# Kernel tuning notes

Measured on AMD Instinct MI355X. Metric: run time of the kernel, lower is better.

Reference implementation:

```python
import jax, jax.numpy as jnp
import numpy as np

D_MODEL = 2048
D_COMPARE = 2048
D_MEMORY = 2048
N_HEADS = 16
KV_HEADS = 4
KV_REPEAT = N_HEADS // KV_HEADS          # 4
C_HD = D_COMPARE // N_HEADS              # 128 compare head dim
M_HD = D_MEMORY // N_HEADS               # 128 memory head dim
TOTAL_OUT = D_COMPARE + KV_HEADS * C_HD + KV_HEADS * M_HD  # 3072


def setup_inputs() -> dict:
    key = jax.random.key(0)
    ks = jax.random.split(key, 5)
    b, t = 2, 2048
    x = jax.random.normal(ks[0], (b, t, D_MODEL), dtype=jnp.float32)
    s_in = 1.0 / np.sqrt(D_MODEL)
    s_out = 1.0 / np.sqrt(D_MEMORY)
    in_w = jax.random.uniform(ks[1], (TOTAL_OUT, D_MODEL), jnp.float32, -s_in, s_in)
    in_b = jax.random.uniform(ks[2], (TOTAL_OUT,), jnp.float32, -s_in, s_in)
    out_w = jax.random.uniform(ks[3], (D_MODEL, D_MEMORY), jnp.float32, -s_out, s_out)
    out_b = jax.random.uniform(ks[4], (D_MODEL,), jnp.float32, -s_out, s_out)
    return {"x": x, "in_w": in_w, "in_b": in_b, "out_w": out_w, "out_b": out_b}


def reference(x, in_w, in_b, out_w, out_b):
    b, t, _ = x.shape
    packed = jnp.einsum("btd,od->bto", x, in_w) + in_b          # [b,t,TOTAL_OUT]
    q, k, v = jnp.split(packed, [D_COMPARE, D_COMPARE + KV_HEADS * C_HD], axis=-1)
    # q: [b, kv, rep, t, hd] -- head h maps to kv group h // KV_REPEAT
    # (torch repeat_interleave on KV head dim == grouped reshape of q heads)
    q = q.reshape(b, t, KV_HEADS, KV_REPEAT, C_HD).transpose(0, 2, 3, 1, 4)
    k = k.reshape(b, t, KV_HEADS, C_HD).transpose(0, 2, 1, 3)   # [b,kv,t,hd]
    v = v.reshape(b, t, KV_HEADS, M_HD).transpose(0, 2, 1, 3)   # [b,kv,t,mhd]
    scale = 1.0 / np.sqrt(C_HD)
    scores = jnp.einsum("bgrqd,bgkd->bgrqk", q, k) * scale      # [b,kv,rep,t,t]
    attn = jax.nn.softmax(scores, axis=-1)
    y = jnp.einsum("bgrqk,bgkd->bgrqd", attn, v)                # [b,kv,rep,t,mhd]
    y = y.transpose(0, 3, 1, 2, 4).reshape(b, t, D_MEMORY)      # heads back in order
    return jnp.einsum("btm,dm->btd", y, out_w) + out_b
```

## Files before the change

### kernel.cpp

```cpp
#include <hip/hip_runtime.h>
#include <hip/hip_bf16.h>
#include <stdint.h>

#define DEV __device__ __forceinline__

typedef __attribute__((ext_vector_type(8))) short bf16x8;
typedef __attribute__((ext_vector_type(4))) float f32x4;
typedef __attribute__((ext_vector_type(16))) float f32x16;
typedef __attribute__((ext_vector_type(4))) unsigned u32x4;

DEV unsigned short f2bf(float f) {
  unsigned u = __builtin_bit_cast(unsigned, f);
  unsigned r = u + 0x7FFF + ((u >> 16) & 1);
  return (unsigned short)(r >> 16);
}

DEV unsigned short f2bfh(float f) {
  __bf16 h = (__bf16)f;
  return __builtin_bit_cast(unsigned short, h);
}

DEV unsigned cvtpk(float lo, float hi) {
  unsigned r;
  asm("v_cvt_pk_bf16_f32 %0, %1, %2" : "=v"(r) : "v"(lo), "v"(hi));
  return r;
}

DEV void plswap(unsigned &a, unsigned &b) {
  asm("v_permlane32_swap_b32 %0, %1" : "+v"(a), "+v"(b));
}

typedef __attribute__((address_space(1))) void gvoid;
typedef __attribute__((address_space(3))) void lvoid;

DEV void g2l16(const void* g, void* l) {
  __builtin_amdgcn_global_load_lds((gvoid*)g, (lvoid*)l, 16, 0, 0);
}

#define MFMA16(a, b, c) __builtin_amdgcn_mfma_f32_16x16x32_bf16(a, b, c, 0, 0, 0)
#define MFMA32(a, b, c) __builtin_amdgcn_mfma_f32_32x32x16_bf16(a, b, c, 0, 0, 0)

__global__ void k_cvt3(const float* __restrict__ x, unsigned short* __restrict__ xo, int nx4,
                       const float* __restrict__ w, unsigned short* __restrict__ wo, int nw4,
                       const float* __restrict__ v, unsigned short* __restrict__ vo, int nv4) {
  int i = blockIdx.x * blockDim.x + threadIdx.x;
  int stride = gridDim.x * blockDim.x;
  int tot = nx4 + nw4 + nv4;
  for (; i < tot; i += stride) {
    const float* src; unsigned short* dst; int j = i;
    if (j < nx4) { src = x; dst = xo; }
    else if ((j -= nx4) < nw4) { src = w; dst = wo; }
    else { j -= nw4; src = v; dst = vo; }
    float4 val = reinterpret_cast<const float4*>(src)[j];
    ushort4 o;
    o.x = f2bf(val.x); o.y = f2bf(val.y); o.z = f2bf(val.z); o.w = f2bf(val.w);
    reinterpret_cast<ushort4*>(dst)[j] = o;
  }
}

template<bool BF16OUT>
__global__ __launch_bounds__(256, 2) void k_gemm(
    const unsigned short* __restrict__ A, const unsigned short* __restrict__ B,
    const float* __restrict__ bias, void* __restrict__ C,
    int M, int N, int K) {
  __shared__ unsigned short As[128 * 32];
  __shared__ unsigned short Bs[128 * 32];
  int tid = threadIdx.x;
  int lane = tid & 63, wid = tid >> 6;
  int bm = blockIdx.y * 128, bn = blockIdx.x * 128;
  int wm = (wid >> 1) * 64, wn = (wid & 1) * 64;
  int row16 = lane & 15, kq = lane >> 4;
  f32x4 acc[4][4] = {};
  int r = tid >> 2, c = (tid & 3) * 8;
  const unsigned short* Ag = A + (size_t)(bm + r) * K + c;
  const unsigned short* Bg = B + (size_t)(bn + r) * K + c;
  for (int k0 = 0; k0 < K; k0 += 32) {
    g2l16(Ag + k0, &As[tid * 8]);
    g2l16(Ag + (size_t)64 * K + k0, &As[2048 + tid * 8]);
    g2l16(Bg + k0, &Bs[tid * 8]);
    g2l16(Bg + (size_t)64 * K + k0, &Bs[2048 + tid * 8]);
    __syncthreads();
    bf16x8 a[4], b[4];
#pragma unroll
    for (int m = 0; m < 4; m++) a[m] = *(const bf16x8*)&As[(wm + m * 16 + row16) * 32 + kq * 8];
#pragma unroll
    for (int n = 0; n < 4; n++) b[n] = *(const bf16x8*)&Bs[(wn + n * 16 + row16) * 32 + kq * 8];
    __builtin_amdgcn_s_setprio(1);
#pragma unroll
    for (int m = 0; m < 4; m++)
#pragma unroll
      for (int n = 0; n < 4; n++)
        acc[m][n] = MFMA16(a[m], b[n], acc[m][n]);
    __builtin_amdgcn_s_setprio(0);
    __syncthreads();
  }
#pragma unroll
  for (int n = 0; n < 4; n++) {
    int col = bn + wn + n * 16 + row16;
    float bv = bias[col];
#pragma unroll
    for (int m = 0; m < 4; m++) {
      int rw = bm + wm + m * 16 + kq * 4;
#pragma unroll
      for (int j = 0; j < 4; j++) {
        float v = acc[m][n][j] + bv;
        if (BF16OUT) ((unsigned short*)C)[(size_t)(rw + j) * N + col] = f2bf(v);
        else         ((float*)C)[(size_t)(rw + j) * N + col] = v;
      }
    }
  }
}

__global__ void k_pack(const unsigned short* __restrict__ packed, unsigned short* __restrict__ attp) {
  __shared__ unsigned short tile[64][136];
  int t = blockIdx.x, g = blockIdx.y;
  int b = g >> 2, kv = g & 3;
  int tid = threadIdx.x;
#pragma unroll
  for (int i = 0; i < 4; i++) {
    int tl = i * 16 + (tid >> 4);
    int d0 = (tid & 15) * 8;
    *(bf16x8*)&tile[tl][d0] =
        *(const bf16x8*)&packed[(size_t)(b * 2048 + t * 64 + tl) * 3072 + 2560 + kv * 128 + d0];
  }
  size_t obase = (size_t)(g * 32 + t) * 32 * 64 * 8;
#pragma unroll
  for (int f = 0; f < 4; f++) {
    int idx = f * 256 + tid;
    int frag = idx >> 6, lane = idx & 63;
    int l31 = lane & 31, h2 = lane >> 5;
    int kb2 = frag >> 3, kc = frag & 7;
    const unsigned short* src = &packed[(size_t)(b * 2048 + t * 64 + kb2 * 32 + l31) * 3072
                                        + 2048 + kv * 128 + (2 * kc + h2) * 8];
    *(bf16x8*)&attp[obase + (size_t)(frag * 64 + lane) * 8] = *(const bf16x8*)src;
  }
  __syncthreads();
#pragma unroll
  for (int f = 0; f < 4; f++) {
    int idx = f * 256 + tid;
    int f16 = idx >> 6, lane = idx & 63;
    int l31 = lane & 31, h2 = lane >> 5;
    int db = f16 >> 2, ks = f16 & 3;
    int d = 32 * db + l31;
    bf16x8 ov;
#pragma unroll
    for (int e = 0; e < 8; e++) ov[e] = (short)tile[(2 * ks + h2) * 8 + e][d];
    *(bf16x8*)&attp[obase + (size_t)((16 + f16) * 64 + lane) * 8] = ov;
  }
}

__global__ __launch_bounds__(512, 2) void k_flash8(
    const unsigned short* __restrict__ packed,
    const unsigned short* __restrict__ attp,
    unsigned short* __restrict__ Y) {
  __shared__ unsigned short S[49152];
  int tid = threadIdx.x, lane = tid & 63, wid = tid >> 6;
  int l31 = lane & 31, hi = lane >> 5;
  int kx = l31 & 15;
  int g = blockIdx.x;
  int s8 = g & 7;
  int b = s8 >> 2, kv = s8 & 3;
  int w = g >> 3;
  int h = kv * 4 + (w & 3);
  int qt = w >> 2;
  size_t prow = (size_t)b * 2048;

  {
    int rr = tid >> 4;
    int cc = ((tid & 15) ^ (rr & 15)) * 8;
    const unsigned short* qg = packed + (prow + qt * 256 + rr) * 3072 + h * 128 + cc;
#pragma unroll
    for (int i = 0; i < 8; i++)
      g2l16(qg + (size_t)i * 32 * 3072, &S[i * 4096 + tid * 8]);
  }
  asm volatile("s_waitcnt vmcnt(0)" ::: "memory");
  __builtin_amdgcn_s_barrier();
  bf16x8 q[8];
  int qrow = wid * 32 + l31;
#pragma unroll
  for (int kc = 0; kc < 8; kc++)
    q[kc] = *(const bf16x8*)&S[qrow * 128 + (((2 * kc + hi) ^ kx) * 8)];
  asm volatile("s_waitcnt lgkmcnt(0)" ::: "memory");
  __builtin_amdgcn_sched_barrier(0);
  __builtin_amdgcn_s_barrier();

  const unsigned short* tstr = attp + (size_t)s8 * 32 * 16384;

  auto stage = [&](int t, int buf) {
    const unsigned short* src = tstr + (size_t)t * 16384 + tid * 8;
    unsigned short* dst = &S[buf * 16384 + tid * 8];
#pragma unroll
    for (int i = 0; i < 4; i++)
      g2l16(src + i * 4096, dst + i * 4096);
  };

  auto qk = [&](int buf, f32x16& s0, f32x16& s1) {
    const unsigned short* B = &S[buf * 16384];
    bf16x8 ak[4];
#pragma unroll
    for (int j = 0; j < 4; j++) ak[j] = *(const bf16x8*)&B[((0 + j) * 64 + lane) * 8];
    __builtin_amdgcn_s_setprio(1);
#pragma unroll
    for (int j = 0; j < 4; j++) s0 = MFMA32(ak[j], q[j], s0);
    __builtin_amdgcn_s_setprio(0);
#pragma unroll
    for (int j = 0; j < 4; j++) ak[j] = *(const bf16x8*)&B[((4 + j) * 64 + lane) * 8];
    __builtin_amdgcn_s_setprio(1);
#pragma unroll
    for (int j = 0; j < 4; j++) s0 = MFMA32(ak[j], q[4 + j], s0);
    __builtin_amdgcn_s_setprio(0);
#pragma unroll
    for (int j = 0; j < 4; j++) ak[j] = *(const bf16x8*)&B[((8 + j) * 64 + lane) * 8];
    __builtin_amdgcn_s_setprio(1);
#pragma unroll
    for (int j = 0; j < 4; j++) s1 = MFMA32(ak[j], q[j], s1);
    __builtin_amdgcn_s_setprio(0);
#pragma unroll
    for (int j = 0; j < 4; j++) ak[j] = *(const bf16x8*)&B[((12 + j) * 64 + lane) * 8];
    __builtin_amdgcn_s_setprio(1);
#pragma unroll
    for (int j = 0; j < 4; j++) s1 = MFMA32(ak[j], q[4 + j], s1);
    __builtin_amdgcn_s_setprio(0);
  };

  stage(0, 0);
  stage(1, 1);
  asm volatile("s_waitcnt vmcnt(0)" ::: "memory");
  __builtin_amdgcn_s_barrier();

  f32x16 stc0 = {}, stc1 = {};
  qk(0, stc0, stc1);

  f32x16 o[4] = {};
  f32x16 ls = {};
  const float sc2 = 0.08838834764831845f * 1.4426950408889634f;
  const float MOFF = 14.f;
  bf16x8 ones;
#pragma unroll
  for (int e = 0; e < 8; e++) ones[e] = (short)0x3F80;

  for (int t = 0; t < 32; t++) {
    int tn2 = t + 2 <= 31 ? t + 2 : 31;

    stage(tn2, (t + 2) % 3);

    f32x16 sn0 = {}, sn1 = {};
    qk((t + 1) % 3, sn0, sn1);

#pragma unroll
    for (int r = 0; r < 16; r++) stc0[r] = exp2f(fmaf(stc0[r], sc2, -MOFF));
#pragma unroll
    for (int r = 0; r < 16; r++) stc1[r] = exp2f(fmaf(stc1[r], sc2, -MOFF));

    bf16x8 pf[4];
    {
      unsigned E0 = cvtpk(stc0[0],  stc0[1]);
      unsigned E1 = cvtpk(stc0[2],  stc0[3]);
      unsigned E2 = cvtpk(stc0[4],  stc0[5]);
      unsigned E3 = cvtpk(stc0[6],  stc0[7]);
      unsigned E4 = cvtpk(stc0[8],  stc0[9]);
      unsigned E5 = cvtpk(stc0[10], stc0[11]);
      unsigned E6 = cvtpk(stc0[12], stc0[13]);
      unsigned E7 = cvtpk(stc0[14], stc0[15]);
      plswap(E0, E2); plswap(E1, E3);
      plswap(E4, E6); plswap(E5, E7);
      pf[0] = __builtin_bit_cast(bf16x8, u32x4{E0, E1, E2, E3});
      pf[1] = __builtin_bit_cast(bf16x8, u32x4{E4, E5, E6, E7});
      unsigned F0 = cvtpk(stc1[0],  stc1[1]);
      unsigned F1 = cvtpk(stc1[2],  stc1[3]);
      unsigned F2 = cvtpk(stc1[4],  stc1[5]);
      unsigned F3 = cvtpk(stc1[6],  stc1[7]);
      unsigned F4 = cvtpk(stc1[8],  stc1[9]);
      unsigned F5 = cvtpk(stc1[10], stc1[11]);
      unsigned F6 = cvtpk(stc1[12], stc1[13]);
      unsigned F7 = cvtpk(stc1[14], stc1[15]);
      plswap(F0, F2); plswap(F1, F3);
      plswap(F4, F6); plswap(F5, F7);
      pf[2] = __builtin_bit_cast(bf16x8, u32x4{F0, F1, F2, F3});
      pf[3] = __builtin_bit_cast(bf16x8, u32x4{F4, F5, F6, F7});
    }

#pragma unroll
    for (int ks = 0; ks < 4; ks++) ls = MFMA32(pf[ks], ones, ls);
    {
      const unsigned short* B = &S[(t % 3) * 16384];
#pragma unroll
      for (int db = 0; db < 4; db++) {
        bf16x8 bv[4];
#pragma unroll
        for (int ks = 0; ks < 4; ks++)
          bv[ks] = *(const bf16x8*)&B[((16 + db * 4 + ks) * 64 + lane) * 8];
        __builtin_amdgcn_s_setprio(1);
#pragma unroll
        for (int ks = 0; ks < 4; ks++) o[db] = MFMA32(pf[ks], bv[ks], o[db]);
        __builtin_amdgcn_s_setprio(0);
      }
    }

    stc0 = sn0;
    stc1 = sn1;

    asm volatile("s_waitcnt vmcnt(0)" ::: "memory");
    __builtin_amdgcn_s_barrier();
  }

#pragma unroll
  for (int r = 0; r < 16; r++) {
    int ql = (r & 3) + 8 * (r >> 2) + 4 * hi;
    float inv = 1.f / ls[r];
    size_t orow = prow + (size_t)qt * 256 + wid * 32 + ql;
#pragma unroll
    for (int db = 0; db < 4; db++)
      Y[orow * 2048 + h * 128 + db * 32 + l31] = f2bfh(o[db][r] * inv);
  }
}

extern "C" void kernel_launch(void* const* d_in, const int* in_sizes, int n_in,
                              void* d_out, int out_size, void* d_ws, size_t ws_size,
                              hipStream_t stream) {
  const float* x     = (const float*)d_in[0];
  const float* in_w  = (const float*)d_in[1];
  const float* in_b  = (const float*)d_in[2];
  const float* out_w = (const float*)d_in[3];
  const float* out_b = (const float*)d_in[4];
  float* out = (float*)d_out;

  unsigned short* xb     = (unsigned short*)d_ws;
  unsigned short* wb     = xb + 8388608;
  unsigned short* owb    = wb + 6291456;
  unsigned short* packed = owb + 4194304;
  unsigned short* y      = packed + 12582912;
  unsigned short* attp   = xb;

  k_cvt3<<<dim3(2048), dim3(256), 0, stream>>>(x, xb, 8388608 / 4,
                                               in_w, wb, 6291456 / 4,
                                               out_w, owb, 4194304 / 4);

  k_gemm<true><<<dim3(24, 32), dim3(256), 0, stream>>>(xb, wb, in_b, packed, 4096, 3072, 2048);
  k_pack<<<dim3(32, 8), dim3(256), 0, stream>>>(packed, attp);
  k_flash8<<<dim3(256), dim3(512), 0, stream>>>(packed, attp, y);
  k_gemm<false><<<dim3(16, 32), dim3(256), 0, stream>>>(y, owb, out_b, out, 4096, 2048, 2048);
}
```

Baseline: 218.1 us.

## Split flash attention KV tile across two wave groups with LDS reduction

```diff
diff --git a/kernel.cpp b/kernel.cpp
--- a/kernel.cpp
+++ b/kernel.cpp
@@ -149,13 +149,16 @@
   }
 }
 
-__global__ __launch_bounds__(512, 2) void k_flash8(
+__global__ __launch_bounds__(512, 4) void k_flash2(
     const unsigned short* __restrict__ packed,
     const unsigned short* __restrict__ attp,
     unsigned short* __restrict__ Y) {
-  __shared__ unsigned short S[49152];
+  __shared__ unsigned short S[2][16384];
+  __shared__ float xr[4][64];
+  __shared__ float axc[4][32];
   int tid = threadIdx.x, lane = tid & 63, wid = tid >> 6;
   int l31 = lane & 31, hi = lane >> 5;
+  int kvh = wid >> 2, qw = wid & 3;
   int kx = l31 & 15;
   int g = blockIdx.x;
   int s8 = g & 7;
@@ -168,18 +171,17 @@
   {
     int rr = tid >> 4;
     int cc = ((tid & 15) ^ (rr & 15)) * 8;
-    const unsigned short* qg = packed + (prow + qt * 256 + rr) * 3072 + h * 128 + cc;
-#pragma unroll
-    for (int i = 0; i < 8; i++)
-      g2l16(qg + (size_t)i * 32 * 3072, &S[i * 4096 + tid * 8]);
+    const unsigned short* qg = packed + (prow + qt * 128 + rr) * 3072 + h * 128 + cc;
+#pragma unroll
+    for (int i = 0; i < 4; i++)
+      g2l16(qg + (size_t)i * 32 * 3072, &S[0][i * 4096 + tid * 8]);
   }
   asm volatile("s_waitcnt vmcnt(0)" ::: "memory");
   __builtin_amdgcn_s_barrier();
   bf16x8 q[8];
-  int qrow = wid * 32 + l31;
 #pragma unroll
   for (int kc = 0; kc < 8; kc++)
-    q[kc] = *(const bf16x8*)&S[qrow * 128 + (((2 * kc + hi) ^ kx) * 8)];
+    q[kc] = *(const bf16x8*)&S[0][(qw * 32 + l31) * 128 + (((2 * kc + hi) ^ kx) * 8)];
   asm volatile("s_waitcnt lgkmcnt(0)" ::: "memory");
   __builtin_amdgcn_sched_barrier(0);
   __builtin_amdgcn_s_barrier();
@@ -188,130 +190,118 @@
 
   auto stage = [&](int t, int buf) {
     const unsigned short* src = tstr + (size_t)t * 16384 + tid * 8;
-    unsigned short* dst = &S[buf * 16384 + tid * 8];
 #pragma unroll
     for (int i = 0; i < 4; i++)
-      g2l16(src + i * 4096, dst + i * 4096);
+      g2l16(src + i * 4096, &S[buf][i * 4096 + tid * 8]);
   };
 
-  auto qk = [&](int buf, f32x16& s0, f32x16& s1) {
-    const unsigned short* B = &S[buf * 16384];
-    bf16x8 ak[4];
-#pragma unroll
-    for (int j = 0; j < 4; j++) ak[j] = *(const bf16x8*)&B[((0 + j) * 64 + lane) * 8];
-    __builtin_amdgcn_s_setprio(1);
-#pragma unroll
-    for (int j = 0; j < 4; j++) s0 = MFMA32(ak[j], q[j], s0);
-    __builtin_amdgcn_s_setprio(0);
-#pragma unroll
-    for (int j = 0; j < 4; j++) ak[j] = *(const bf16x8*)&B[((4 + j) * 64 + lane) * 8];
-    __builtin_amdgcn_s_setprio(1);
-#pragma unroll
-    for (int j = 0; j < 4; j++) s0 = MFMA32(ak[j], q[4 + j], s0);
-    __builtin_amdgcn_s_setprio(0);
-#pragma unroll
-    for (int j = 0; j < 4; j++) ak[j] = *(const bf16x8*)&B[((8 + j) * 64 + lane) * 8];
-    __builtin_amdgcn_s_setprio(1);
-#pragma unroll
-    for (int j = 0; j < 4; j++) s1 = MFMA32(ak[j], q[j], s1);
-    __builtin_amdgcn_s_setprio(0);
-#pragma unroll
-    for (int j = 0; j < 4; j++) ak[j] = *(const bf16x8*)&B[((12 + j) * 64 + lane) * 8];
-    __builtin_amdgcn_s_setprio(1);
-#pragma unroll
-    for (int j = 0; j < 4; j++) s1 = MFMA32(ak[j], q[4 + j], s1);
-    __builtin_amdgcn_s_setprio(0);
-  };
-
   stage(0, 0);
-  stage(1, 1);
   asm volatile("s_waitcnt vmcnt(0)" ::: "memory");
   __builtin_amdgcn_s_barrier();
 
-  f32x16 stc0 = {}, stc1 = {};
-  qk(0, stc0, stc1);
-
   f32x16 o[4] = {};
-  f32x16 ls = {};
+  float lr = 0.f;
   const float sc2 = 0.08838834764831845f * 1.4426950408889634f;
   const float MOFF = 14.f;
-  bf16x8 ones;
-#pragma unroll
-  for (int e = 0; e < 8; e++) ones[e] = (short)0x3F80;
 
   for (int t = 0; t < 32; t++) {
-    int tn2 = t + 2 <= 31 ? t + 2 : 31;
-
-    stage(tn2, (t + 2) % 3);
-
-    f32x16 sn0 = {}, sn1 = {};
-    qk((t + 1) % 3, sn0, sn1);
-
-#pragma unroll
-    for (int r = 0; r < 16; r++) stc0[r] = exp2f(fmaf(stc0[r], sc2, -MOFF));
-#pragma unroll
-    for (int r = 0; r < 16; r++) stc1[r] = exp2f(fmaf(stc1[r], sc2, -MOFF));
-
-    bf16x8 pf[4];
+    int tn = t < 31 ? t + 1 : 31;
+    stage(tn, (t + 1) & 1);
+
+    const unsigned short* B = &S[t & 1][0];
+
+    f32x16 st = {};
     {
-      unsigned E0 = cvtpk(stc0[0],  stc0[1]);
-      unsigned E1 = cvtpk(stc0[2],  stc0[3]);
-      unsigned E2 = cvtpk(stc0[4],  stc0[5]);
-      unsigned E3 = cvtpk(stc0[6],  stc0[7]);
-      unsigned E4 = cvtpk(stc0[8],  stc0[9]);
-      unsigned E5 = cvtpk(stc0[10], stc0[11]);
-      unsigned E6 = cvtpk(stc0[12], stc0[13]);
-      unsigned E7 = cvtpk(stc0[14], stc0[15]);
+      bf16x8 ak[4];
+#pragma unroll
+      for (int j = 0; j < 4; j++)
+        ak[j] = *(const bf16x8*)&B[((kvh * 8 + j) * 64 + lane) * 8];
+      __builtin_amdgcn_s_setprio(1);
+#pragma unroll
+      for (int j = 0; j < 4; j++) st = MFMA32(ak[j], q[j], st);
+      __builtin_amdgcn_s_setprio(0);
+#pragma unroll
+      for (int j = 0; j < 4; j++)
+        ak[j] = *(const bf16x8*)&B[((kvh * 8 + 4 + j) * 64 + lane) * 8];
+      __builtin_amdgcn_s_setprio(1);
+#pragma unroll
+      for (int j = 0; j < 4; j++) st = MFMA32(ak[j], q[4 + j], st);
+      __builtin_amdgcn_s_setprio(0);
+    }
+
+#pragma unroll
+    for (int r = 0; r < 16; r++) st[r] = exp2f(fmaf(st[r], sc2, -MOFF));
+    {
+      float s0 = (st[0] + st[1]) + (st[2] + st[3]);
+      float s1 = (st[4] + st[5]) + (st[6] + st[7]);
+      float s2 = (st[8] + st[9]) + (st[10] + st[11]);
+      float s3 = (st[12] + st[13]) + (st[14] + st[15]);
+      float rs = (s0 + s1) + (s2 + s3);
+      rs += __shfl_xor(rs, 32);
+      lr += rs;
+    }
+
+    bf16x8 pf[2];
+    {
+      unsigned E0 = cvtpk(st[0],  st[1]);
+      unsigned E1 = cvtpk(st[2],  st[3]);
+      unsigned E2 = cvtpk(st[4],  st[5]);
+      unsigned E3 = cvtpk(st[6],  st[7]);
+      unsigned E4 = cvtpk(st[8],  st[9]);
+      unsigned E5 = cvtpk(st[10], st[11]);
+      unsigned E6 = cvtpk(st[12], st[13]);
+      unsigned E7 = cvtpk(st[14], st[15]);
       plswap(E0, E2); plswap(E1, E3);
       plswap(E4, E6); plswap(E5, E7);
       pf[0] = __builtin_bit_cast(bf16x8, u32x4{E0, E1, E2, E3});
       pf[1] = __builtin_bit_cast(bf16x8, u32x4{E4, E5, E6, E7});
-      unsigned F0 = cvtpk(stc1[0],  stc1[1]);
-      unsigned F1 = cvtpk(stc1[2],  stc1[3]);
-      unsigned F2 = cvtpk(stc1[4],  stc1[5]);
-      unsigned F3 = cvtpk(stc1[6],  stc1[7]);
-      unsigned F4 = cvtpk(stc1[8],  stc1[9]);
-      unsigned F5 = cvtpk(stc1[10], stc1[11]);
-      unsigned F6 = cvtpk(stc1[12], stc1[13]);
-      unsigned F7 = cvtpk(stc1[14], stc1[15]);
-      plswap(F0, F2); plswap(F1, F3);
-      plswap(F4, F6); plswap(F5, F7);
-      pf[2] = __builtin_bit_cast(bf16x8, u32x4{F0, F1, F2, F3});
-      pf[3] = __builtin_bit_cast(bf16x8, u32x4{F4, F5, F6, F7});
-    }
-
-#pragma unroll
-    for (int ks = 0; ks < 4; ks++) ls = MFMA32(pf[ks], ones, ls);
-    {
-      const unsigned short* B = &S[(t % 3) * 16384];
-#pragma unroll
-      for (int db = 0; db < 4; db++) {
-        bf16x8 bv[4];
-#pragma unroll
-        for (int ks = 0; ks < 4; ks++)
-          bv[ks] = *(const bf16x8*)&B[((16 + db * 4 + ks) * 64 + lane) * 8];
-        __builtin_amdgcn_s_setprio(1);
-#pragma unroll
-        for (int ks = 0; ks < 4; ks++) o[db] = MFMA32(pf[ks], bv[ks], o[db]);
-        __builtin_amdgcn_s_setprio(0);
-      }
-    }
-
-    stc0 = sn0;
-    stc1 = sn1;
+    }
+
+#pragma unroll
+    for (int db = 0; db < 4; db++) {
+      bf16x8 bv0 = *(const bf16x8*)&B[((16 + db * 4 + 2 * kvh + 0) * 64 + lane) * 8];
+      bf16x8 bv1 = *(const bf16x8*)&B[((16 + db * 4 + 2 * kvh + 1) * 64 + lane) * 8];
+      __builtin_amdgcn_s_setprio(1);
+      o[db] = MFMA32(pf[0], bv0, o[db]);
+      o[db] = MFMA32(pf[1], bv1, o[db]);
+      __builtin_amdgcn_s_setprio(0);
+    }
 
     asm volatile("s_waitcnt vmcnt(0)" ::: "memory");
     __builtin_amdgcn_s_barrier();
   }
 
-#pragma unroll
-  for (int r = 0; r < 16; r++) {
-    int ql = (r & 3) + 8 * (r >> 2) + 4 * hi;
-    float inv = 1.f / ls[r];
-    size_t orow = prow + (size_t)qt * 256 + wid * 32 + ql;
+  float* xO = (float*)&S[0][0];
+  if (kvh) {
+    float* dst = xO + qw * 4096 + lane * 64;
 #pragma unroll
     for (int db = 0; db < 4; db++)
-      Y[orow * 2048 + h * 128 + db * 32 + l31] = f2bfh(o[db][r] * inv);
+#pragma unroll
+      for (int r4 = 0; r4 < 4; r4++) {
+        f32x4 v = { o[db][r4 * 4 + 0], o[db][r4 * 4 + 1],
+                    o[db][r4 * 4 + 2], o[db][r4 * 4 + 3] };
+        *(f32x4*)&dst[db * 16 + r4 * 4] = v;
+      }
+    xr[qw][lane] = lr;
+  }
+  __builtin_amdgcn_s_barrier();
+  if (!kvh) {
+    const float* src = xO + qw * 4096 + lane * 64;
+#pragma unroll
+    for (int db = 0; db < 4; db++)
+#pragma unroll
+      for (int r = 0; r < 16; r++) o[db][r] += src[db * 16 + r];
+    lr += xr[qw][lane];
+    axc[qw][l31] = lr;
+#pragma unroll
+    for (int r = 0; r < 16; r++) {
+      int ql = (r & 3) + 8 * (r >> 2) + 4 * hi;
+      float inv = 1.f / axc[qw][ql];
+      size_t orow = prow + (size_t)qt * 128 + qw * 32 + ql;
+#pragma unroll
+      for (int db = 0; db < 4; db++)
+        Y[orow * 2048 + h * 128 + db * 32 + l31] = f2bfh(o[db][r] * inv);
+    }
   }
 }
 
@@ -338,6 +328,6 @@
 
   k_gemm<true><<<dim3(24, 32), dim3(256), 0, stream>>>(xb, wb, in_b, packed, 4096, 3072, 2048);
   k_pack<<<dim3(32, 8), dim3(256), 0, stream>>>(packed, attp);
-  k_flash8<<<dim3(256), dim3(512), 0, stream>>>(packed, attp, y);
+  k_flash2<<<dim3(512), dim3(512), 0, stream>>>(packed, attp, y);
   k_gemm<false><<<dim3(16, 32), dim3(256), 0, stream>>>(y, owb, out_b, out, 4096, 2048, 2048);
 }
```

Result: slower. 243.5 us (+11.6%).

## Load V fragments directly to registers and compute row sums with VALU

Applied to the files above, without the earlier changes.

```diff
diff --git a/kernel.cpp b/kernel.cpp
--- a/kernel.cpp
+++ b/kernel.cpp
@@ -149,11 +149,12 @@
   }
 }
 
-__global__ __launch_bounds__(512, 2) void k_flash8(
+__global__ __launch_bounds__(512, 2) void k_flash9(
     const unsigned short* __restrict__ packed,
     const unsigned short* __restrict__ attp,
     unsigned short* __restrict__ Y) {
-  __shared__ unsigned short S[49152];
+  __shared__ unsigned short S[3][8192];
+  __shared__ float axc[8][32];
   int tid = threadIdx.x, lane = tid & 63, wid = tid >> 6;
   int l31 = lane & 31, hi = lane >> 5;
   int kx = l31 & 15;
@@ -165,37 +166,42 @@
   int qt = w >> 2;
   size_t prow = (size_t)b * 2048;
 
+  bf16x8 q[8];
   {
-    int rr = tid >> 4;
-    int cc = ((tid & 15) ^ (rr & 15)) * 8;
-    const unsigned short* qg = packed + (prow + qt * 256 + rr) * 3072 + h * 128 + cc;
-#pragma unroll
-    for (int i = 0; i < 8; i++)
-      g2l16(qg + (size_t)i * 32 * 3072, &S[i * 4096 + tid * 8]);
-  }
-  asm volatile("s_waitcnt vmcnt(0)" ::: "memory");
-  __builtin_amdgcn_s_barrier();
-  bf16x8 q[8];
-  int qrow = wid * 32 + l31;
-#pragma unroll
-  for (int kc = 0; kc < 8; kc++)
-    q[kc] = *(const bf16x8*)&S[qrow * 128 + (((2 * kc + hi) ^ kx) * 8)];
-  asm volatile("s_waitcnt lgkmcnt(0)" ::: "memory");
-  __builtin_amdgcn_sched_barrier(0);
-  __builtin_amdgcn_s_barrier();
+    unsigned short* Qs = &S[0][0];
+#pragma unroll
+    for (int p = 0; p < 2; p++) {
+      int rr = tid >> 4;
+      int cc = ((tid & 15) ^ (rr & 15)) * 8;
+      const unsigned short* qg = packed + (prow + qt * 256 + p * 128 + rr) * 3072 + h * 128 + cc;
+#pragma unroll
+      for (int i = 0; i < 4; i++)
+        g2l16(qg + (size_t)i * 32 * 3072, &Qs[i * 4096 + tid * 8]);
+      asm volatile("s_waitcnt vmcnt(0)" ::: "memory");
+      __builtin_amdgcn_s_barrier();
+      if ((wid >> 2) == p) {
+        int qr = (wid & 3) * 32 + l31;
+#pragma unroll
+        for (int kc = 0; kc < 8; kc++)
+          q[kc] = *(const bf16x8*)&Qs[qr * 128 + (((2 * kc + hi) ^ kx) * 8)];
+      }
+      asm volatile("s_waitcnt lgkmcnt(0)" ::: "memory");
+      __builtin_amdgcn_sched_barrier(0);
+      __builtin_amdgcn_s_barrier();
+    }
+  }
 
   const unsigned short* tstr = attp + (size_t)s8 * 32 * 16384;
-
-  auto stage = [&](int t, int buf) {
+  const bf16x8* vst = (const bf16x8*)attp;
+
+  auto stageK = [&](int t, int buf) {
     const unsigned short* src = tstr + (size_t)t * 16384 + tid * 8;
-    unsigned short* dst = &S[buf * 16384 + tid * 8];
-#pragma unroll
-    for (int i = 0; i < 4; i++)
-      g2l16(src + i * 4096, dst + i * 4096);
+    g2l16(src, &S[buf][tid * 8]);
+    g2l16(src + 4096, &S[buf][4096 + tid * 8]);
   };
 
   auto qk = [&](int buf, f32x16& s0, f32x16& s1) {
-    const unsigned short* B = &S[buf * 16384];
+    const unsigned short* B = &S[buf][0];
     bf16x8 ak[4];
 #pragma unroll
     for (int j = 0; j < 4; j++) ak[j] = *(const bf16x8*)&B[((0 + j) * 64 + lane) * 8];
@@ -223,26 +229,28 @@
     __builtin_amdgcn_s_setprio(0);
   };
 
-  stage(0, 0);
-  stage(1, 1);
-  asm volatile("s_waitcnt vmcnt(0)" ::: "memory");
+  stageK(0, 0);
+  stageK(1, 1);
+  bf16x8 bv[16];
+#pragma unroll
+  for (int f = 0; f < 16; f++)
+    bv[f] = vst[(size_t)(s8 * 32 + 0) * 2048 + 1024 + f * 64 + lane];
+  asm volatile("s_waitcnt vmcnt(16)" ::: "memory");
   __builtin_amdgcn_s_barrier();
 
   f32x16 stc0 = {}, stc1 = {};
   qk(0, stc0, stc1);
 
   f32x16 o[4] = {};
-  f32x16 ls = {};
+  float lr = 0.f;
   const float sc2 = 0.08838834764831845f * 1.4426950408889634f;
   const float MOFF = 14.f;
-  bf16x8 ones;
-#pragma unroll
-  for (int e = 0; e < 8; e++) ones[e] = (short)0x3F80;
 
   for (int t = 0; t < 32; t++) {
-    int tn2 = t + 2 <= 31 ? t + 2 : 31;
-
-    stage(tn2, (t + 2) % 3);
+    int tn  = t < 31 ? t + 1 : 31;
+    int tn2 = t < 30 ? t + 2 : 31;
+
+    stageK(tn2, (t + 2) % 3);
 
     f32x16 sn0 = {}, sn1 = {};
     qk((t + 1) % 3, sn0, sn1);
@@ -251,6 +259,17 @@
     for (int r = 0; r < 16; r++) stc0[r] = exp2f(fmaf(stc0[r], sc2, -MOFF));
 #pragma unroll
     for (int r = 0; r < 16; r++) stc1[r] = exp2f(fmaf(stc1[r], sc2, -MOFF));
+    {
+      float s0 = 0.f, s1 = 0.f;
+#pragma unroll
+      for (int r = 0; r < 16; r += 4) {
+        s0 += (stc0[r] + stc0[r + 1]) + (stc0[r + 2] + stc0[r + 3]);
+        s1 += (stc1[r] + stc1[r + 1]) + (stc1[r + 2] + stc1[r + 3]);
+      }
+      float rs = s0 + s1;
+      rs += __shfl_xor(rs, 32);
+      lr += rs;
+    }
 
     bf16x8 pf[4];
     {
@@ -280,34 +299,30 @@
       pf[3] = __builtin_bit_cast(bf16x8, u32x4{F4, F5, F6, F7});
     }
 
-#pragma unroll
-    for (int ks = 0; ks < 4; ks++) ls = MFMA32(pf[ks], ones, ls);
-    {
-      const unsigned short* B = &S[(t % 3) * 16384];
-#pragma unroll
-      for (int db = 0; db < 4; db++) {
-        bf16x8 bv[4];
-#pragma unroll
-        for (int ks = 0; ks < 4; ks++)
-          bv[ks] = *(const bf16x8*)&B[((16 + db * 4 + ks) * 64 + lane) * 8];
-        __builtin_amdgcn_s_setprio(1);
-#pragma unroll
-        for (int ks = 0; ks < 4; ks++) o[db] = MFMA32(pf[ks], bv[ks], o[db]);
-        __builtin_amdgcn_s_setprio(0);
-      }
+    size_t vb = (size_t)(s8 * 32 + tn) * 2048 + 1024;
+#pragma unroll
+    for (int db = 0; db < 4; db++) {
+      __builtin_amdgcn_s_setprio(1);
+#pragma unroll
+      for (int ks = 0; ks < 4; ks++) o[db] = MFMA32(pf[ks], bv[db * 4 + ks], o[db]);
+      __builtin_amdgcn_s_setprio(0);
+#pragma unroll
+      for (int ks = 0; ks < 4; ks++) bv[db * 4 + ks] = vst[vb + (db * 4 + ks) * 64 + lane];
     }
 
     stc0 = sn0;
     stc1 = sn1;
 
-    asm volatile("s_waitcnt vmcnt(0)" ::: "memory");
+    asm volatile("s_waitcnt vmcnt(16)" ::: "memory");
     __builtin_amdgcn_s_barrier();
   }
-
+  asm volatile("s_waitcnt vmcnt(0)" ::: "memory");
+
+  axc[wid][l31] = lr;
 #pragma unroll
   for (int r = 0; r < 16; r++) {
     int ql = (r & 3) + 8 * (r >> 2) + 4 * hi;
-    float inv = 1.f / ls[r];
+    float inv = 1.f / axc[wid][ql];
     size_t orow = prow + (size_t)qt * 256 + wid * 32 + ql;
 #pragma unroll
     for (int db = 0; db < 4; db++)
@@ -338,6 +353,6 @@
 
   k_gemm<true><<<dim3(24, 32), dim3(256), 0, stream>>>(xb, wb, in_b, packed, 4096, 3072, 2048);
   k_pack<<<dim3(32, 8), dim3(256), 0, stream>>>(packed, attp);
-  k_flash8<<<dim3(256), dim3(512), 0, stream>>>(packed, attp, y);
+  k_flash9<<<dim3(256), dim3(512), 0, stream>>>(packed, attp, y);
   k_gemm<false><<<dim3(16, 32), dim3(256), 0, stream>>>(y, owb, out_b, out, 4096, 2048, 2048);
 }
```

Result: slower. 268.7 us (+23.2%).

## Split flash waves into two phase-offset groups over a four-buffer KV ring

Applied to the files above, without the earlier changes.

```diff
diff --git a/kernel.cpp b/kernel.cpp
--- a/kernel.cpp
+++ b/kernel.cpp
@@ -149,11 +149,11 @@
   }
 }
 
-__global__ __launch_bounds__(512, 2) void k_flash8(
+__global__ __launch_bounds__(512, 1) void k_flashS(
     const unsigned short* __restrict__ packed,
     const unsigned short* __restrict__ attp,
     unsigned short* __restrict__ Y) {
-  __shared__ unsigned short S[49152];
+  __shared__ unsigned short S[4][16384];
   int tid = threadIdx.x, lane = tid & 63, wid = tid >> 6;
   int l31 = lane & 31, hi = lane >> 5;
   int kx = l31 & 15;
@@ -165,13 +165,14 @@
   int qt = w >> 2;
   size_t prow = (size_t)b * 2048;
 
+  unsigned short* Sf = &S[0][0];
   {
     int rr = tid >> 4;
     int cc = ((tid & 15) ^ (rr & 15)) * 8;
     const unsigned short* qg = packed + (prow + qt * 256 + rr) * 3072 + h * 128 + cc;
 #pragma unroll
     for (int i = 0; i < 8; i++)
-      g2l16(qg + (size_t)i * 32 * 3072, &S[i * 4096 + tid * 8]);
+      g2l16(qg + (size_t)i * 32 * 3072, &Sf[i * 4096 + tid * 8]);
   }
   asm volatile("s_waitcnt vmcnt(0)" ::: "memory");
   __builtin_amdgcn_s_barrier();
@@ -179,7 +180,7 @@
   int qrow = wid * 32 + l31;
 #pragma unroll
   for (int kc = 0; kc < 8; kc++)
-    q[kc] = *(const bf16x8*)&S[qrow * 128 + (((2 * kc + hi) ^ kx) * 8)];
+    q[kc] = *(const bf16x8*)&Sf[qrow * 128 + (((2 * kc + hi) ^ kx) * 8)];
   asm volatile("s_waitcnt lgkmcnt(0)" ::: "memory");
   __builtin_amdgcn_sched_barrier(0);
   __builtin_amdgcn_s_barrier();
@@ -188,14 +189,14 @@
 
   auto stage = [&](int t, int buf) {
     const unsigned short* src = tstr + (size_t)t * 16384 + tid * 8;
-    unsigned short* dst = &S[buf * 16384 + tid * 8];
+    unsigned short* dst = &S[buf][tid * 8];
 #pragma unroll
     for (int i = 0; i < 4; i++)
       g2l16(src + i * 4096, dst + i * 4096);
   };
 
   auto qk = [&](int buf, f32x16& s0, f32x16& s1) {
-    const unsigned short* B = &S[buf * 16384];
+    const unsigned short* B = &S[buf][0];
     bf16x8 ak[4];
 #pragma unroll
     for (int j = 0; j < 4; j++) ak[j] = *(const bf16x8*)&B[((0 + j) * 64 + lane) * 8];
@@ -221,6 +222,63 @@
 #pragma unroll
     for (int j = 0; j < 4; j++) s1 = MFMA32(ak[j], q[4 + j], s1);
     __builtin_amdgcn_s_setprio(0);
+  };
+
+  const float sc2 = 0.08838834764831845f * 1.4426950408889634f;
+  const float MOFF = 14.f;
+
+  auto smcvt = [&](f32x16& a0, f32x16& a1, bf16x8* pf) {
+#pragma unroll
+    for (int r = 0; r < 16; r++) a0[r] = exp2f(fmaf(a0[r], sc2, -MOFF));
+#pragma unroll
+    for (int r = 0; r < 16; r++) a1[r] = exp2f(fmaf(a1[r], sc2, -MOFF));
+    unsigned E0 = cvtpk(a0[0],  a0[1]);
+    unsigned E1 = cvtpk(a0[2],  a0[3]);
+    unsigned E2 = cvtpk(a0[4],  a0[5]);
+    unsigned E3 = cvtpk(a0[6],  a0[7]);
+    unsigned E4 = cvtpk(a0[8],  a0[9]);
+    unsigned E5 = cvtpk(a0[10], a0[11]);
+    unsigned E6 = cvtpk(a0[12], a0[13]);
+    unsigned E7 = cvtpk(a0[14], a0[15]);
+    plswap(E0, E2); plswap(E1, E3);
+    plswap(E4, E6); plswap(E5, E7);
+    pf[0] = __builtin_bit_cast(bf16x8, u32x4{E0, E1, E2, E3});
+    pf[1] = __builtin_bit_cast(bf16x8, u32x4{E4, E5, E6, E7});
+    unsigned F0 = cvtpk(a1[0],  a1[1]);
+    unsigned F1 = cvtpk(a1[2],  a1[3]);
+    unsigned F2 = cvtpk(a1[4],  a1[5]);
+    unsigned F3 = cvtpk(a1[6],  a1[7]);
+    unsigned F4 = cvtpk(a1[8],  a1[9]);
+    unsigned F5 = cvtpk(a1[10], a1[11]);
+    unsigned F6 = cvtpk(a1[12], a1[13]);
+    unsigned F7 = cvtpk(a1[14], a1[15]);
+    plswap(F0, F2); plswap(F1, F3);
+    plswap(F4, F6); plswap(F5, F7);
+    pf[2] = __builtin_bit_cast(bf16x8, u32x4{F0, F1, F2, F3});
+    pf[3] = __builtin_bit_cast(bf16x8, u32x4{F4, F5, F6, F7});
+  };
+
+  f32x16 o[4] = {};
+  f32x16 ls = {};
+  bf16x8 ones;
+#pragma unroll
+  for (int e = 0; e < 8; e++) ones[e] = (short)0x3F80;
+
+  auto pv = [&](int buf, bf16x8* pf) {
+#pragma unroll
+    for (int ks = 0; ks < 4; ks++) ls = MFMA32(pf[ks], ones, ls);
+    const unsigned short* B = &S[buf][0];
+#pragma unroll
+    for (int db = 0; db < 4; db++) {
+      bf16x8 bv[4];
+#pragma unroll
+      for (int ks = 0; ks < 4; ks++)
+        bv[ks] = *(const bf16x8*)&B[((16 + db * 4 + ks) * 64 + lane) * 8];
+      __builtin_amdgcn_s_setprio(1);
+#pragma unroll
+      for (int ks = 0; ks < 4; ks++) o[db] = MFMA32(pf[ks], bv[ks], o[db]);
+      __builtin_amdgcn_s_setprio(0);
+    }
   };
 
   stage(0, 0);
@@ -228,81 +286,34 @@
   asm volatile("s_waitcnt vmcnt(0)" ::: "memory");
   __builtin_amdgcn_s_barrier();
 
+  bool isA = wid < 4;
   f32x16 stc0 = {}, stc1 = {};
-  qk(0, stc0, stc1);
-
-  f32x16 o[4] = {};
-  f32x16 ls = {};
-  const float sc2 = 0.08838834764831845f * 1.4426950408889634f;
-  const float MOFF = 14.f;
-  bf16x8 ones;
-#pragma unroll
-  for (int e = 0; e < 8; e++) ones[e] = (short)0x3F80;
+  bf16x8 pfB[4];
+  if (isA) qk(0, stc0, stc1);
 
   for (int t = 0; t < 32; t++) {
     int tn2 = t + 2 <= 31 ? t + 2 : 31;
-
-    stage(tn2, (t + 2) % 3);
-
-    f32x16 sn0 = {}, sn1 = {};
-    qk((t + 1) % 3, sn0, sn1);
-
-#pragma unroll
-    for (int r = 0; r < 16; r++) stc0[r] = exp2f(fmaf(stc0[r], sc2, -MOFF));
-#pragma unroll
-    for (int r = 0; r < 16; r++) stc1[r] = exp2f(fmaf(stc1[r], sc2, -MOFF));
-
-    bf16x8 pf[4];
-    {
-      unsigned E0 = cvtpk(stc0[0],  stc0[1]);
-      unsigned E1 = cvtpk(stc0[2],  stc0[3]);
-      unsigned E2 = cvtpk(stc0[4],  stc0[5]);
-      unsigned E3 = cvtpk(stc0[6],  stc0[7]);
-      unsigned E4 = cvtpk(stc0[8],  stc0[9]);
-      unsigned E5 = cvtpk(stc0[10], stc0[11]);
-      unsigned E6 = cvtpk(stc0[12], stc0[13]);
-      unsigned E7 = cvtpk(stc0[14], stc0[15]);
-      plswap(E0, E2); plswap(E1, E3);
-      plswap(E4, E6); plswap(E5, E7);
-      pf[0] = __builtin_bit_cast(bf16x8, u32x4{E0, E1, E2, E3});
-      pf[1] = __builtin_bit_cast(bf16x8, u32x4{E4, E5, E6, E7});
-      unsigned F0 = cvtpk(stc1[0],  stc1[1]);
-      unsigned F1 = cvtpk(stc1[2],  stc1[3]);
-      unsigned F2 = cvtpk(stc1[4],  stc1[5]);
-      unsigned F3 = cvtpk(stc1[6],  stc1[7]);
-      unsigned F4 = cvtpk(stc1[8],  stc1[9]);
-      unsigned F5 = cvtpk(stc1[10], stc1[11]);
-      unsigned F6 = cvtpk(stc1[12], stc1[13]);
-      unsigned F7 = cvtpk(stc1[14], stc1[15]);
-      plswap(F0, F2); plswap(F1, F3);
-      plswap(F4, F6); plswap(F5, F7);
-      pf[2] = __builtin_bit_cast(bf16x8, u32x4{F0, F1, F2, F3});
-      pf[3] = __builtin_bit_cast(bf16x8, u32x4{F4, F5, F6, F7});
+    stage(tn2, (t + 2) & 3);
+
+    if (isA) {
+      f32x16 sn0 = {}, sn1 = {};
+      qk((t + 1) & 3, sn0, sn1);
+      bf16x8 pfA[4];
+      smcvt(stc0, stc1, pfA);
+      pv(t & 3, pfA);
+      stc0 = sn0;
+      stc1 = sn1;
+    } else {
+      if (t > 0) pv((t - 1) & 3, pfB);
+      f32x16 sb0 = {}, sb1 = {};
+      qk(t & 3, sb0, sb1);
+      smcvt(sb0, sb1, pfB);
     }
-
-#pragma unroll
-    for (int ks = 0; ks < 4; ks++) ls = MFMA32(pf[ks], ones, ls);
-    {
-      const unsigned short* B = &S[(t % 3) * 16384];
-#pragma unroll
-      for (int db = 0; db < 4; db++) {
-        bf16x8 bv[4];
-#pragma unroll
-        for (int ks = 0; ks < 4; ks++)
-          bv[ks] = *(const bf16x8*)&B[((16 + db * 4 + ks) * 64 + lane) * 8];
-        __builtin_amdgcn_s_setprio(1);
-#pragma unroll
-        for (int ks = 0; ks < 4; ks++) o[db] = MFMA32(pf[ks], bv[ks], o[db]);
-        __builtin_amdgcn_s_setprio(0);
-      }
-    }
-
-    stc0 = sn0;
-    stc1 = sn1;
 
     asm volatile("s_waitcnt vmcnt(0)" ::: "memory");
     __builtin_amdgcn_s_barrier();
   }
+  if (!isA) pv(3, pfB);
 
 #pragma unroll
   for (int r = 0; r < 16; r++) {
@@ -338,6 +349,6 @@
 
   k_gemm<true><<<dim3(24, 32), dim3(256), 0, stream>>>(xb, wb, in_b, packed, 4096, 3072, 2048);
   k_pack<<<dim3(32, 8), dim3(256), 0, stream>>>(packed, attp);
-  k_flash8<<<dim3(256), dim3(512), 0, stream>>>(packed, attp, y);
+  k_flashS<<<dim3(256), dim3(512), 0, stream>>>(packed, attp, y);
   k_gemm<false><<<dim3(16, 32), dim3(256), 0, stream>>>(y, owb, out_b, out, 4096, 2048, 2048);
 }
```

Measured after the change: 213.8 us. 2.0% less time.
